# Kernel tuning notes

Measured on AMD Instinct MI355X. Metric: run time of the kernel, lower is better.

## Reference

```python
import jax, jax.numpy as jnp
import numpy as np

EPS = 1e-6


def setup_inputs() -> dict:
    key = jax.random.key(0)
    k1, k2, k3, k4 = jax.random.split(key, 4)
    B, H, J, K = 32, 8, 8192, 128
    memory = jax.random.normal(k1, (B, J, K), dtype=jnp.float32)
    keys = jax.random.normal(k2, (B, H, K), dtype=jnp.float32)
    strengths = jax.random.normal(k3, (B, H, 1), dtype=jnp.float32)
    mask = jax.random.uniform(k4, (B, H, K), dtype=jnp.float32)
    return {"memory": memory, "keys": keys, "strengths": strengths, "mask": mask}


def reference(memory, keys, strengths, mask):
    # Faithful math: masked_keys = mask*keys; masked_memory[i,h,j,k] = mask[i,h,k]*memory[i,j,k]
    # projections[i,h,j] = sum_k mask^2 * keys * memory  (mask appears in both operands)
    # We fold mask^2 into the contractions to avoid materializing [i,h,j,k].
    mask2 = mask * mask                                   # [B,H,K]
    projections = jnp.einsum('ihk,ijk->ihj', mask2 * keys, memory)
    keys_norm = jnp.linalg.norm(mask * keys, axis=-1)     # [B,H]
    # ||masked_memory||[i,h,j] = sqrt(sum_k mask^2 * memory^2)
    memory_norm = jnp.sqrt(jnp.einsum('ihk,ijk->ihj', mask2, memory * memory))
    norm = keys_norm[..., None] * memory_norm             # [B,H,J]
    similarity = projections / (norm + EPS)
    sharp = similarity * jax.nn.softplus(strengths)       # strengths [B,H,1] broadcasts
    return jax.nn.softmax(sharp, axis=-1)
```

## Files before the change

### kernel.cpp

```cpp
#include <hip/hip_runtime.h>
#include <math.h>

constexpr int B_ = 32;
constexpr int H_ = 8;
constexpr int J_ = 8192;
constexpr int K_ = 128;
constexpr float EPS_ = 1e-6f;

constexpr int SBLK = 64;
constexpr int JPB  = J_ / SBLK;
constexpr int RPI  = 8;
constexpr int ITERS = JPB / RPI;

template <int CTRL>
__device__ __forceinline__ float dpp_add(float x) {
  int v = __builtin_amdgcn_update_dpp(0, __float_as_int(x), CTRL, 0xF, 0xF, true);
  return x + __int_as_float(v);
}

__device__ __forceinline__ float red16(float x) {
  x = dpp_add<0xB1>(x);
  x = dpp_add<0x4E>(x);
  x = dpp_add<0x141>(x);
  x = dpp_add<0x140>(x);
  return x;
}

__device__ __forceinline__ float dot4f(const float4 a, const float4 b, float acc) {
  acc = fmaf(a.x, b.x, acc);
  acc = fmaf(a.y, b.y, acc);
  acc = fmaf(a.z, b.z, acc);
  acc = fmaf(a.w, b.w, acc);
  return acc;
}

__global__ __launch_bounds__(256, 4) void cw_main(
    const float* __restrict__ memory, const float* __restrict__ keys,
    const float* __restrict__ strengths, const float* __restrict__ mask,
    float* __restrict__ out)
{
  const int bid  = blockIdx.x;
  const int i    = bid >> 6;
  const int jb   = bid & 63;
  const int t    = threadIdx.x;
  const int wave = t >> 6;
  const int lane = t & 63;
  const int grp  = lane >> 4;
  const int sub  = lane & 15;
  const int hs   = (wave >> 1) << 2;
  const int hl   = sub & 3;
  const int myh  = hs + hl;

  const float4* keyv = (const float4*)(keys + (size_t)i * H_ * K_);
  const float4* mskv = (const float4*)(mask + (size_t)i * H_ * K_);
  float4 cA[4][2];
  float4 cB[4][2];
  float kn[4];
  #pragma unroll
  for (int hh = 0; hh < 4; ++hh) {
    const int h = hs + hh;
    float knp = 0.0f;
    #pragma unroll
    for (int c = 0; c < 2; ++c) {
      const float4 kv = keyv[h * 32 + c * 16 + sub];
      const float4 mv = mskv[h * 32 + c * 16 + sub];
      float4 b, a;
      b.x = mv.x * mv.x; b.y = mv.y * mv.y; b.z = mv.z * mv.z; b.w = mv.w * mv.w;
      a.x = b.x * kv.x;  a.y = b.y * kv.y;  a.z = b.z * kv.z;  a.w = b.w * kv.w;
      cB[hh][c] = b;
      cA[hh][c] = a;
      knp = dot4f(a, kv, knp);
    }
    kn[hh] = red16(knp);
  }
  float kn2 = kn[0];
  #pragma unroll
  for (int hh = 1; hh < 4; ++hh) if (hl == hh) kn2 = kn[hh];
  const float knorm = sqrtf(kn2);
  const float st = strengths[i * H_ + myh];
  const float sp = fmaxf(st, 0.0f) + log1pf(expf(-fabsf(st)));

  const int jrow0 = (wave & 1) * 4 + grp;
  const int j0    = jb * JPB + jrow0;
  const float4* rowv = (const float4*)(memory + ((size_t)i * J_ + j0) * K_);

  float4 m0 = rowv[sub];
  float4 m1 = rowv[sub + 16];

  #pragma unroll 1
  for (int it = 0; it < ITERS; ++it) {
    const int nx = (it + 1 < ITERS) ? (it + 1) : 0;
    const float4* nr = rowv + (size_t)nx * 256;
    const float4 n0v = nr[sub];
    const float4 n1v = nr[sub + 16];

    float4 sq0, sq1;
    sq0.x = m0.x * m0.x; sq0.y = m0.y * m0.y; sq0.z = m0.z * m0.z; sq0.w = m0.w * m0.w;
    sq1.x = m1.x * m1.x; sq1.y = m1.y * m1.y; sq1.z = m1.z * m1.z; sq1.w = m1.w * m1.w;

    float p[4], nn[4];
    #pragma unroll
    for (int hh = 0; hh < 4; ++hh) {
      float a = m0.x * cA[hh][0].x;
      a = fmaf(m0.y, cA[hh][0].y, a);
      a = fmaf(m0.z, cA[hh][0].z, a);
      a = fmaf(m0.w, cA[hh][0].w, a);
      a = dot4f(m1, cA[hh][1], a);
      p[hh] = a;
      float b = sq0.x * cB[hh][0].x;
      b = fmaf(sq0.y, cB[hh][0].y, b);
      b = fmaf(sq0.z, cB[hh][0].z, b);
      b = fmaf(sq0.w, cB[hh][0].w, b);
      b = dot4f(sq1, cB[hh][1], b);
      nn[hh] = b;
    }

    #pragma unroll
    for (int hh = 0; hh < 4; ++hh) {
      p[hh]  = red16(p[hh]);
      nn[hh] = red16(nn[hh]);
    }

    if (sub < 4) {
      float pp = p[0], qq = nn[0];
      #pragma unroll
      for (int hh = 1; hh < 4; ++hh) {
        if (hl == hh) { pp = p[hh]; qq = nn[hh]; }
      }
      const float mnorm = sqrtf(qq);
      const float sharp = pp / (knorm * mnorm + EPS_) * sp;
      const int j = jb * JPB + it * RPI + jrow0;
      out[((size_t)(i * H_ + myh)) * J_ + j] = sharp;
    }

    m0 = n0v;
    m1 = n1v;
  }
}

__global__ __launch_bounds__(1024) void cw_softmax(float* __restrict__ out)
{
  const int row = blockIdx.x;
  float4* pv = (float4*)(out + (size_t)row * J_);
  const int t = threadIdx.x;
  const int wave = t >> 6, lane = t & 63;

  float4 v0 = pv[t];
  float4 v1 = pv[t + 1024];
  float mx = fmaxf(fmaxf(fmaxf(v0.x, v0.y), fmaxf(v0.z, v0.w)),
                   fmaxf(fmaxf(v1.x, v1.y), fmaxf(v1.z, v1.w)));
  #pragma unroll
  for (int o = 32; o > 0; o >>= 1) mx = fmaxf(mx, __shfl_xor(mx, o, 64));
  __shared__ float sm[16];
  __shared__ float ss[16];
  if (lane == 0) sm[wave] = mx;
  __syncthreads();
  mx = sm[lane & 15];
  #pragma unroll
  for (int o = 8; o > 0; o >>= 1) mx = fmaxf(mx, __shfl_xor(mx, o, 64));

  v0.x = expf(v0.x - mx); v0.y = expf(v0.y - mx);
  v0.z = expf(v0.z - mx); v0.w = expf(v0.w - mx);
  v1.x = expf(v1.x - mx); v1.y = expf(v1.y - mx);
  v1.z = expf(v1.z - mx); v1.w = expf(v1.w - mx);
  float sum = ((v0.x + v0.y) + (v0.z + v0.w)) + ((v1.x + v1.y) + (v1.z + v1.w));
  #pragma unroll
  for (int o = 32; o > 0; o >>= 1) sum += __shfl_xor(sum, o, 64);
  if (lane == 0) ss[wave] = sum;
  __syncthreads();
  sum = ss[lane & 15];
  #pragma unroll
  for (int o = 8; o > 0; o >>= 1) sum += __shfl_xor(sum, o, 64);
  const float inv = 1.0f / sum;

  v0.x *= inv; v0.y *= inv; v0.z *= inv; v0.w *= inv;
  v1.x *= inv; v1.y *= inv; v1.z *= inv; v1.w *= inv;
  pv[t] = v0;
  pv[t + 1024] = v1;
}

extern "C" void kernel_launch(void* const* d_in, const int* in_sizes, int n_in,
                              void* d_out, int out_size, void* d_ws, size_t ws_size,
                              hipStream_t stream) {
  const float* memory    = (const float*)d_in[0];
  const float* keys      = (const float*)d_in[1];
  const float* strengths = (const float*)d_in[2];
  const float* mask      = (const float*)d_in[3];
  float* out = (float*)d_out;

  (void)d_ws; (void)ws_size;

  cw_main<<<B_ * SBLK, 256, 0, stream>>>(memory, keys, strengths, mask, out);
  cw_softmax<<<B_ * H_, 1024, 0, stream>>>(out);
}
```

Baseline: 206.5 us.

## Process 16 rows per iteration with 8-lane groups and shorter reductions

Each row is now handled by 8 lanes, each holding 16 elements, instead of 16 lanes holding 8. Each wave therefore covers twice as many memory rows per iteration, with half as many iterations. The cross-lane reduction drops one DPP step (red16 becomes red8), which cuts shuffle and reduction overhead per row. In exchange, register use grows (cA/cB become 4x4 float4 arrays plus a larger prefetch buffer), so launch bounds drop to 2 blocks per SIMD and occupancy may fall.

After: 210.1 us. No clear change (+1.7%).

```diff
diff --git a/kernel.cpp b/kernel.cpp
--- a/kernel.cpp
+++ b/kernel.cpp
@@ -9,7 +9,7 @@
 
 constexpr int SBLK = 64;
 constexpr int JPB  = J_ / SBLK;
-constexpr int RPI  = 8;
+constexpr int RPI  = 16;
 constexpr int ITERS = JPB / RPI;
 
 template <int CTRL>
@@ -18,11 +18,10 @@
   return x + __int_as_float(v);
 }
 
-__device__ __forceinline__ float red16(float x) {
+__device__ __forceinline__ float red8(float x) {
   x = dpp_add<0xB1>(x);
   x = dpp_add<0x4E>(x);
   x = dpp_add<0x141>(x);
-  x = dpp_add<0x140>(x);
   return x;
 }
 
@@ -34,7 +33,7 @@
   return acc;
 }
 
-__global__ __launch_bounds__(256, 4) void cw_main(
+__global__ __launch_bounds__(256, 2) void cw_main(
     const float* __restrict__ memory, const float* __restrict__ keys,
     const float* __restrict__ strengths, const float* __restrict__ mask,
     float* __restrict__ out)
@@ -45,25 +44,25 @@
   const int t    = threadIdx.x;
   const int wave = t >> 6;
   const int lane = t & 63;
-  const int grp  = lane >> 4;
-  const int sub  = lane & 15;
+  const int grp  = lane >> 3;
+  const int sub  = lane & 7;
   const int hs   = (wave >> 1) << 2;
   const int hl   = sub & 3;
   const int myh  = hs + hl;
 
   const float4* keyv = (const float4*)(keys + (size_t)i * H_ * K_);
   const float4* mskv = (const float4*)(mask + (size_t)i * H_ * K_);
-  float4 cA[4][2];
-  float4 cB[4][2];
+  float4 cA[4][4];
+  float4 cB[4][4];
   float kn[4];
   #pragma unroll
   for (int hh = 0; hh < 4; ++hh) {
     const int h = hs + hh;
     float knp = 0.0f;
     #pragma unroll
-    for (int c = 0; c < 2; ++c) {
-      const float4 kv = keyv[h * 32 + c * 16 + sub];
-      const float4 mv = mskv[h * 32 + c * 16 + sub];
+    for (int c = 0; c < 4; ++c) {
+      const float4 kv = keyv[h * 32 + c * 8 + sub];
+      const float4 mv = mskv[h * 32 + c * 8 + sub];
       float4 b, a;
       b.x = mv.x * mv.x; b.y = mv.y * mv.y; b.z = mv.z * mv.z; b.w = mv.w * mv.w;
       a.x = b.x * kv.x;  a.y = b.y * kv.y;  a.z = b.z * kv.z;  a.w = b.w * kv.w;
@@ -71,7 +70,7 @@
       cA[hh][c] = a;
       knp = dot4f(a, kv, knp);
     }
-    kn[hh] = red16(knp);
+    kn[hh] = red8(knp);
   }
   float kn2 = kn[0];
   #pragma unroll
@@ -80,45 +79,46 @@
   const float st = strengths[i * H_ + myh];
   const float sp = fmaxf(st, 0.0f) + log1pf(expf(-fabsf(st)));
 
-  const int jrow0 = (wave & 1) * 4 + grp;
+  const int jrow0 = (wave & 1) * 8 + grp;
   const int j0    = jb * JPB + jrow0;
   const float4* rowv = (const float4*)(memory + ((size_t)i * J_ + j0) * K_);
 
-  float4 m0 = rowv[sub];
-  float4 m1 = rowv[sub + 16];
+  float4 m[4];
+  #pragma unroll
+  for (int c = 0; c < 4; ++c) m[c] = rowv[c * 8 + sub];
 
   #pragma unroll 1
   for (int it = 0; it < ITERS; ++it) {
     const int nx = (it + 1 < ITERS) ? (it + 1) : 0;
-    const float4* nr = rowv + (size_t)nx * 256;
-    const float4 n0v = nr[sub];
-    const float4 n1v = nr[sub + 16];
+    const float4* nr = rowv + (size_t)nx * 512;
+    float4 nf[4];
+    #pragma unroll
+    for (int c = 0; c < 4; ++c) nf[c] = nr[c * 8 + sub];
 
-    float4 sq0, sq1;
-    sq0.x = m0.x * m0.x; sq0.y = m0.y * m0.y; sq0.z = m0.z * m0.z; sq0.w = m0.w * m0.w;
-    sq1.x = m1.x * m1.x; sq1.y = m1.y * m1.y; sq1.z = m1.z * m1.z; sq1.w = m1.w * m1.w;
+    float4 sq[4];
+    #pragma unroll
+    for (int c = 0; c < 4; ++c) {
+      sq[c].x = m[c].x * m[c].x; sq[c].y = m[c].y * m[c].y;
+      sq[c].z = m[c].z * m[c].z; sq[c].w = m[c].w * m[c].w;
+    }
 
     float p[4], nn[4];
     #pragma unroll
     for (int hh = 0; hh < 4; ++hh) {
-      float a = m0.x * cA[hh][0].x;
-      a = fmaf(m0.y, cA[hh][0].y, a);
-      a = fmaf(m0.z, cA[hh][0].z, a);
-      a = fmaf(m0.w, cA[hh][0].w, a);
-      a = dot4f(m1, cA[hh][1], a);
+      float a = 0.0f, b = 0.0f;
+      #pragma unroll
+      for (int c = 0; c < 4; ++c) {
+        a = dot4f(m[c],  cA[hh][c], a);
+        b = dot4f(sq[c], cB[hh][c], b);
+      }
       p[hh] = a;
-      float b = sq0.x * cB[hh][0].x;
-      b = fmaf(sq0.y, cB[hh][0].y, b);
-      b = fmaf(sq0.z, cB[hh][0].z, b);
-      b = fmaf(sq0.w, cB[hh][0].w, b);
-      b = dot4f(sq1, cB[hh][1], b);
       nn[hh] = b;
     }
 
     #pragma unroll
     for (int hh = 0; hh < 4; ++hh) {
-      p[hh]  = red16(p[hh]);
-      nn[hh] = red16(nn[hh]);
+      p[hh]  = red8(p[hh]);
+      nn[hh] = red8(nn[hh]);
     }
 
     if (sub < 4) {
@@ -133,8 +133,8 @@
       out[((size_t)(i * H_ + myh)) * J_ + j] = sharp;
     }
 
-    m0 = n0v;
-    m1 = n1v;
+    #pragma unroll
+    for (int c = 0; c < 4; ++c) m[c] = nf[c];
   }
 }
 
```
